# Kernel optimization log

Measured on AMD Instinct MI355X. Metric: run time of the kernel, lower is better.

Reference implementation:

```python
import jax, jax.numpy as jnp
import numpy as np

DIM = 128
HEADS = 4
DIM_HEAD = 32
HIDDEN = HEADS * DIM_HEAD  # 128
EPS = 1e-5


def setup_inputs() -> dict:
    key = jax.random.key(0)
    ks = jax.random.split(key, 5)
    x = jax.random.normal(ks[0], (32, DIM, 64, 64), dtype=jnp.float32)
    # 1x1 convs are channel matmuls
    Wqkv = jax.random.normal(ks[1], (HIDDEN * 3, DIM), dtype=jnp.float32) * (1.0 / np.sqrt(DIM))
    Wout = jax.random.normal(ks[2], (DIM, HIDDEN), dtype=jnp.float32) * (1.0 / np.sqrt(HIDDEN))
    bout = jnp.zeros((DIM,), dtype=jnp.float32)
    ln_w = jnp.ones((DIM,), dtype=jnp.float32)
    ln_b = jnp.zeros((DIM,), dtype=jnp.float32)
    return {"x": x, "Wqkv": Wqkv, "Wout": Wout, "bout": bout, "ln_w": ln_w, "ln_b": ln_b}


def reference(x, Wqkv, Wout, bout, ln_w, ln_b):
    b, c, h, w = x.shape
    n = h * w
    xf = x.reshape(b, c, n)  # b c n
    qkv = jnp.einsum('oc,bcn->bon', Wqkv, xf)  # b (3*hidden) n
    q, k, v = jnp.split(qkv, 3, axis=1)
    # b (h d) n -> b h d n
    q = q.reshape(b, HEADS, DIM_HEAD, n)
    k = k.reshape(b, HEADS, DIM_HEAD, n)
    v = v.reshape(b, HEADS, DIM_HEAD, n)
    q = jax.nn.softmax(q, axis=-2)  # over feature dim d
    k = jax.nn.softmax(k, axis=-1)  # over spatial dim n
    context = jnp.einsum('bhdn,bhen->bhde', k, v)
    out = jnp.einsum('bhde,bhdn->bhen', context, q)  # b h e n
    out = out.reshape(b, HIDDEN, n)
    out = jnp.einsum('oc,bcn->bon', Wout, out) + bout[None, :, None]
    out = out.reshape(b, DIM, h, w)
    # LayerNorm2d over channel dim, biased variance
    mean = jnp.mean(out, axis=1, keepdims=True)
    var = jnp.var(out, axis=1, keepdims=True)
    out = (out - mean) / jnp.sqrt(var + EPS) * ln_w[None, :, None, None] + ln_b[None, :, None, None]
    return out
```

## Files before the change

kernel.cpp:

```cpp
#include <hip/hip_runtime.h>
#include <stdint.h>


constexpr int B_   = 32;
constexpr int C_   = 128;
constexpr int N_   = 4096;
constexpr int NSUB = 8;
constexpr int TPB_ = 8;

using short8  = __attribute__((ext_vector_type(8))) short;
using short4v = __attribute__((ext_vector_type(4))) short;
using float4v = __attribute__((ext_vector_type(4))) float;

__device__ __forceinline__ unsigned short bf16_rne(float f) {
    union { float f; uint32_t u; } v; v.f = f;
    uint32_t u = v.u;
    u += 0x7FFFu + ((u >> 16) & 1u);
    return (unsigned short)(u >> 16);
}

constexpr size_t OFF_SP   = 0;
constexpr size_t OFF_CTXP = 131072;
constexpr size_t OFF_WBIG = 4325376;
constexpr size_t OFF_QSM  = 5373952;

__global__ __launch_bounds__(1024) void k1_qkv(const float* __restrict__ x,
                                               const float* __restrict__ Wqkv,
                                               unsigned short* __restrict__ qsm,
                                               float* __restrict__ ctx_part,
                                               float* __restrict__ S_part) {
    __shared__ __align__(16) unsigned short xs0[64 * 136];
    __shared__ __align__(16) unsigned short xs1[64 * 136];
    __shared__ __align__(16) unsigned short ek[128 * 72];
    __shared__ __align__(16) unsigned short vsh[128 * 72];

    const int b    = blockIdx.y;
    const int tblk = blockIdx.x;
    const int tid  = threadIdx.x;

    const int lane = tid & 63;
    const int wv   = tid >> 6;
    const int l15  = lane & 15;
    const int quad = lane >> 4;

    const float4v zero = {0.f, 0.f, 0.f, 0.f};

    short8 wfa[8];
    if (wv < 12) {
        const float* wqp = Wqkv + (wv * 32 + l15) * C_ + quad * 8;
        #pragma unroll
        for (int kk = 0; kk < 4; kk++) {
            float4v a0 = *(const float4v*)(wqp + kk * 32);
            float4v a1 = *(const float4v*)(wqp + kk * 32 + 4);
            float4v b0 = *(const float4v*)(wqp + 16 * C_ + kk * 32);
            float4v b1 = *(const float4v*)(wqp + 16 * C_ + kk * 32 + 4);
            short8 lo, hi;
            #pragma unroll
            for (int j = 0; j < 4; j++) {
                lo[j]     = (short)bf16_rne(a0[j]);
                lo[4 + j] = (short)bf16_rne(a1[j]);
                hi[j]     = (short)bf16_rne(b0[j]);
                hi[4 + j] = (short)bf16_rne(b1[j]);
            }
            wfa[kk]     = lo;
            wfa[4 + kk] = hi;
        }
    }

    const int sid = tid & 255;
    const int snl = sid & 63;
    const int scg = sid >> 6;
    const float* xbase = x + ((size_t)b * C_ + (size_t)scg * 32) * N_ + snl;
    float xv[32];
    short8 c16[4];
    auto load_x = [&](int s) {
        const float* xp = xbase + (tblk * NSUB + s) * 64;
        #pragma unroll
        for (int i = 0; i < 32; i++) xv[i] = xp[(size_t)i * N_];
    };
    auto conv_x = [&]() {
        #pragma unroll
        for (int ii = 0; ii < 4; ii++) {
            short8 v8;
            #pragma unroll
            for (int j = 0; j < 8; j++) v8[j] = (short)bf16_rne(xv[ii * 8 + j]);
            c16[ii] = v8;
        }
    };
    auto store_c = [&](unsigned short* xs) {
        unsigned short* dst = &xs[snl * 136 + scg * 32];
        #pragma unroll
        for (int ii = 0; ii < 4; ii++) *(short8*)(dst + ii * 8) = c16[ii];
    };

    if (wv >= 12) {
        load_x(0); conv_x(); store_c(xs0);
        load_x(1);
    }
    unsigned short* xs_cur = xs0;
    unsigned short* xs_nxt = xs1;

    float4v cacc = zero;
    float sk0[4] = {0.f, 0.f, 0.f, 0.f};
    float sk1[4] = {0.f, 0.f, 0.f, 0.f};
    const int ch  = wv >> 2;
    const int cdt = (wv >> 1) & 1;
    const int cet = wv & 1;

    for (int s = 0; s < NSUB; s++) {
        const int ns = (tblk * NSUB + s) * 64;
        __syncthreads();

        if (wv < 12) {
            #pragma unroll
            for (int ct = 0; ct < 4; ct++) {
                short8 bfx[4];
                #pragma unroll
                for (int kk = 0; kk < 4; kk++)
                    bfx[kk] = *(const short8*)&xs_cur[(ct * 16 + l15) * 136 + kk * 32 + quad * 8];
                float4v acc0 = zero, acc1 = zero;
                #pragma unroll
                for (int kk = 0; kk < 4; kk++) {
                    acc0 = __builtin_amdgcn_mfma_f32_16x16x32_bf16(wfa[kk],     bfx[kk], acc0, 0, 0, 0);
                    acc1 = __builtin_amdgcn_mfma_f32_16x16x32_bf16(wfa[4 + kk], bfx[kk], acc1, 0, 0, 0);
                }
                const int ncol = ct * 16 + l15;
                if (wv < 4) {
                    float e0[4], e1[4], z = 0.f;
                    #pragma unroll
                    for (int r = 0; r < 4; r++) {
                        e0[r] = __expf(acc0[r]); e1[r] = __expf(acc1[r]);
                        z += e0[r] + e1[r];
                    }
                    z += __shfl_xor(z, 16, 64);
                    z += __shfl_xor(z, 32, 64);
                    const float iz = 1.0f / z;
                    unsigned short* qp = qsm + ((size_t)b * N_ + ns + ncol) * C_ + wv * 32 + quad * 4;
                    short4v s0, s1;
                    #pragma unroll
                    for (int r = 0; r < 4; r++) {
                        s0[r] = (short)bf16_rne(e0[r] * iz);
                        s1[r] = (short)bf16_rne(e1[r] * iz);
                    }
                    *(short4v*)qp = s0;
                    *(short4v*)(qp + 16) = s1;
                } else if (wv < 8) {
                    const int row0 = (wv - 4) * 32 + quad * 4;
                    #pragma unroll
                    for (int r = 0; r < 4; r++) {
                        const float e0v = __expf(acc0[r]);
                        const float e1v = __expf(acc1[r]);
                        sk0[r] += e0v;
                        sk1[r] += e1v;
                        ek[(row0 + r) * 72 + ncol]      = bf16_rne(e0v);
                        ek[(row0 + 16 + r) * 72 + ncol] = bf16_rne(e1v);
                    }
                } else {
                    const int row0 = (wv - 8) * 32 + quad * 4;
                    #pragma unroll
                    for (int r = 0; r < 4; r++) {
                        vsh[(row0 + r) * 72 + ncol]      = bf16_rne(acc0[r]);
                        vsh[(row0 + 16 + r) * 72 + ncol] = bf16_rne(acc1[r]);
                    }
                }
            }
        } else {
            if (s + 1 < NSUB) { conv_x(); store_c(xs_nxt); }
            if (s + 2 < NSUB) load_x(s + 2);
        }
        __syncthreads();

        {
            const unsigned short* ap = &ek[(ch * 32 + cdt * 16 + l15) * 72 + quad * 8];
            const unsigned short* bp = &vsh[(ch * 32 + cet * 16 + l15) * 72 + quad * 8];
            #pragma unroll
            for (int kk = 0; kk < 2; kk++) {
                short8 a  = *(const short8*)(ap + kk * 32);
                short8 bb = *(const short8*)(bp + kk * 32);
                cacc = __builtin_amdgcn_mfma_f32_16x16x32_bf16(a, bb, cacc, 0, 0, 0);
            }
        }
        { unsigned short* t = xs_cur; xs_cur = xs_nxt; xs_nxt = t; }
    }

    {
        float* cp = ctx_part + ((size_t)(b * TPB_ + tblk) << 12)
                  + ((ch * 32 + cdt * 16 + quad * 4) * 32 + cet * 16 + l15);
        #pragma unroll
        for (int r = 0; r < 4; r++) cp[r * 32] = cacc[r];
    }
    if (wv >= 4 && wv < 8) {
        const int srow = (wv - 4) * 32 + quad * 4;
        float* sp = S_part + (size_t)(b * TPB_ + tblk) * 128;
        #pragma unroll
        for (int r = 0; r < 4; r++) {
            float a0 = sk0[r], a1 = sk1[r];
            a0 += __shfl_xor(a0, 1, 64); a0 += __shfl_xor(a0, 2, 64);
            a0 += __shfl_xor(a0, 4, 64); a0 += __shfl_xor(a0, 8, 64);
            a1 += __shfl_xor(a1, 1, 64); a1 += __shfl_xor(a1, 2, 64);
            a1 += __shfl_xor(a1, 4, 64); a1 += __shfl_xor(a1, 8, 64);
            if (l15 == 0) { sp[srow + r] = a0; sp[srow + 16 + r] = a1; }
        }
    }
}

__global__ __launch_bounds__(512) void k2_fused(const float* __restrict__ ctx_part,
                                                const float* __restrict__ S_part,
                                                const float* __restrict__ Wout,
                                                unsigned short* __restrict__ wbig) {
    __shared__ float Sinv[128];
    __shared__ __align__(16) unsigned short ctxb[128 * 40];
    const int b   = blockIdx.x;
    const int tid = threadIdx.x;

    if (tid < 128) {
        float s = 0.f;
        #pragma unroll
        for (int t = 0; t < TPB_; t++)
            s += S_part[(size_t)(b * TPB_ + t) * 128 + tid];
        Sinv[tid] = 1.0f / s;
    }
    __syncthreads();

    #pragma unroll
    for (int i = 0; i < 8; i++) {
        const int ei = i * 512 + tid;
        float v = 0.f;
        #pragma unroll
        for (int t = 0; t < TPB_; t++)
            v += ctx_part[((size_t)(b * TPB_ + t) << 12) + ei];
        ctxb[(ei >> 5) * 40 + (ei & 31)] = bf16_rne(v * Sinv[ei >> 5]);
    }
    __syncthreads();

    const int lane = tid & 63, wv = tid >> 6, l15 = lane & 15, quad = lane >> 4;
    const float4v zero = {0.f, 0.f, 0.f, 0.f};

    short8 a4[4];
    {
        const float* wop = Wout + (wv * 16 + l15) * C_ + quad * 8;
        #pragma unroll
        for (int h = 0; h < 4; h++) {
            float4v f0 = *(const float4v*)(wop + h * 32);
            float4v f1 = *(const float4v*)(wop + h * 32 + 4);
            short8 w;
            #pragma unroll
            for (int j = 0; j < 4; j++) {
                w[j]     = (short)bf16_rne(f0[j]);
                w[4 + j] = (short)bf16_rne(f1[j]);
            }
            a4[h] = w;
        }
    }

    unsigned short* wb = wbig + (size_t)b * (C_ * C_);
    #pragma unroll
    for (int ht = 0; ht < 8; ht++) {
        const int h_ = ht >> 1;
        short8 bb = *(const short8*)&ctxb[(h_ * 32 + (ht & 1) * 16 + l15) * 40 + quad * 8];
        float4v c4 = __builtin_amdgcn_mfma_f32_16x16x32_bf16(a4[h_], bb, zero, 0, 0, 0);
        const int c     = wv * 4 + (ht >> 1);
        const int quadp = (ht & 1) * 2 + (l15 >> 3);
        #pragma unroll
        for (int r = 0; r < 4; r++)
            wb[((c * 64 + quadp * 16 + quad * 4 + r) << 3) + (l15 & 7)] = bf16_rne(c4[r]);
    }
}

__global__ __launch_bounds__(512) void k3_out(const unsigned short* __restrict__ qsm,
                                              const unsigned short* __restrict__ wbig,
                                              const float* __restrict__ bout,
                                              const float* __restrict__ lnw,
                                              const float* __restrict__ lnb,
                                              float* __restrict__ out) {
    __shared__ __align__(16) unsigned short wls[16384];
    __shared__ float lnp[384];

    const int b    = blockIdx.y;
    const int tseg = blockIdx.x;
    const int tid  = threadIdx.x;

    const int lane = tid & 63, wv = tid >> 6, l15 = lane & 15, quad = lane >> 4;
    const int nl = wv * 16 + l15;

    const float4v zero = {0.f, 0.f, 0.f, 0.f};
    const size_t n0base = (size_t)tseg * 256;

    short8 st[4];
    {
        const short8* src = (const short8*)(wbig + (size_t)b * (C_ * C_));
        #pragma unroll
        for (int i = 0; i < 4; i++) st[i] = src[i * 512 + tid];
    }
    if (tid < 128) {
        lnp[tid]       = bout[tid];
        lnp[128 + tid] = lnw[tid];
        lnp[256 + tid] = lnb[tid];
    }
    short8 bq[4], bqn[4];
    {
        const unsigned short* qp = qsm + ((size_t)b * N_ + n0base + nl) * C_ + quad * 8;
        #pragma unroll
        for (int kk = 0; kk < 4; kk++) bq[kk] = *(const short8*)(qp + kk * 32);
    }
    #pragma unroll
    for (int i = 0; i < 4; i++)
        *(short8*)&wls[(i * 512 + tid) * 8] = st[i];
    __syncthreads();

    #pragma unroll
    for (int t = 0; t < 2; t++) {
        const size_t n = n0base + t * 128 + nl;
        if (t == 0) {
            const unsigned short* qp = qsm + ((size_t)b * N_ + n0base + 128 + nl) * C_ + quad * 8;
            #pragma unroll
            for (int kk = 0; kk < 4; kk++) bqn[kk] = *(const short8*)(qp + kk * 32);
        }

        float4v acc[8];
        #pragma unroll
        for (int ot = 0; ot < 8; ot++) {
            float4v a = zero;
            #pragma unroll
            for (int kk = 0; kk < 4; kk++) {
                short8 w = *(const short8*)&wls[((ot * 4 + kk) * 64 + lane) * 8];
                a = __builtin_amdgcn_mfma_f32_16x16x32_bf16(w, bq[kk], a, 0, 0, 0);
            }
            acc[ot] = a;
        }

        float sum = 0.f, sq = 0.f;
        #pragma unroll
        for (int ot = 0; ot < 8; ot++) {
            #pragma unroll
            for (int r = 0; r < 4; r++) {
                const int o = ot * 16 + quad * 4 + r;
                const float y = acc[ot][r] + lnp[o];
                acc[ot][r] = y;
                sum += y; sq += y * y;
            }
        }
        sum += __shfl_xor(sum, 16, 64);
        sum += __shfl_xor(sum, 32, 64);
        sq  += __shfl_xor(sq, 16, 64);
        sq  += __shfl_xor(sq, 32, 64);
        const float mean = sum * (1.0f / 128.0f);
        const float var  = sq * (1.0f / 128.0f) - mean * mean;
        const float rstd = rsqrtf(var + 1e-5f);

        #pragma unroll
        for (int ot = 0; ot < 8; ot++) {
            #pragma unroll
            for (int r = 0; r < 4; r++) {
                const int o = ot * 16 + quad * 4 + r;
                out[((size_t)b * C_ + o) * N_ + n] = (acc[ot][r] - mean) * rstd * lnp[128 + o] + lnp[256 + o];
            }
        }

        #pragma unroll
        for (int kk = 0; kk < 4; kk++) bq[kk] = bqn[kk];
    }
}

extern "C" void kernel_launch(void* const* d_in, const int* in_sizes, int n_in,
                              void* d_out, int out_size, void* d_ws, size_t ws_size,
                              hipStream_t stream) {
    const float* x    = (const float*)d_in[0];
    const float* Wqkv = (const float*)d_in[1];
    const float* Wout = (const float*)d_in[2];
    const float* bout = (const float*)d_in[3];
    const float* lnw  = (const float*)d_in[4];
    const float* lnb  = (const float*)d_in[5];
    float* out = (float*)d_out;

    char* ws = (char*)d_ws;
    float* S_part        = (float*)(ws + OFF_SP);
    float* ctx_part      = (float*)(ws + OFF_CTXP);
    unsigned short* wbig = (unsigned short*)(ws + OFF_WBIG);
    unsigned short* qsm  = (unsigned short*)(ws + OFF_QSM);

    k1_qkv<<<dim3(TPB_, B_), 1024, 0, stream>>>(x, Wqkv, qsm, ctx_part, S_part);
    k2_fused<<<B_, 512, 0, stream>>>(ctx_part, S_part, Wout, wbig);
    k3_out<<<dim3(16, B_), 512, 0, stream>>>(qsm, wbig, bout, lnw, lnb, out);
}
```

Before: 157.5 us.

## Retile QKV projection so each wave computes 64 rows by 32 columns

```diff
diff --git a/kernel.cpp b/kernel.cpp
--- a/kernel.cpp
+++ b/kernel.cpp
@@ -20,9 +20,9 @@
 }
 
 constexpr size_t OFF_SP   = 0;
-constexpr size_t OFF_CTXP = 131072;
-constexpr size_t OFF_WBIG = 4325376;
-constexpr size_t OFF_QSM  = 5373952;
+constexpr size_t OFF_CTXP = 262144;
+constexpr size_t OFF_WBIG = 4456448;
+constexpr size_t OFF_QSM  = 5505024;
 
 __global__ __launch_bounds__(1024) void k1_qkv(const float* __restrict__ x,
                                                const float* __restrict__ Wqkv,
@@ -45,25 +45,26 @@
 
     const float4v zero = {0.f, 0.f, 0.f, 0.f};
 
-    short8 wfa[8];
+    const int rg = wv >> 1;
+    const int cg = wv & 1;
+
+    short8 wfa[16];
     if (wv < 12) {
-        const float* wqp = Wqkv + (wv * 32 + l15) * C_ + quad * 8;
-        #pragma unroll
-        for (int kk = 0; kk < 4; kk++) {
-            float4v a0 = *(const float4v*)(wqp + kk * 32);
-            float4v a1 = *(const float4v*)(wqp + kk * 32 + 4);
-            float4v b0 = *(const float4v*)(wqp + 16 * C_ + kk * 32);
-            float4v b1 = *(const float4v*)(wqp + 16 * C_ + kk * 32 + 4);
-            short8 lo, hi;
-            #pragma unroll
-            for (int j = 0; j < 4; j++) {
-                lo[j]     = (short)bf16_rne(a0[j]);
-                lo[4 + j] = (short)bf16_rne(a1[j]);
-                hi[j]     = (short)bf16_rne(b0[j]);
-                hi[4 + j] = (short)bf16_rne(b1[j]);
-            }
-            wfa[kk]     = lo;
-            wfa[4 + kk] = hi;
+        const float* wqp = Wqkv + ((size_t)(rg * 64 + l15)) * C_ + quad * 8;
+        #pragma unroll
+        for (int rt = 0; rt < 4; rt++) {
+            #pragma unroll
+            for (int kk = 0; kk < 4; kk++) {
+                float4v f0 = *(const float4v*)(wqp + rt * 16 * C_ + kk * 32);
+                float4v f1 = *(const float4v*)(wqp + rt * 16 * C_ + kk * 32 + 4);
+                short8 w;
+                #pragma unroll
+                for (int j = 0; j < 4; j++) {
+                    w[j]     = (short)bf16_rne(f0[j]);
+                    w[4 + j] = (short)bf16_rne(f1[j]);
+                }
+                wfa[rt * 4 + kk] = w;
+            }
         }
     }
 
@@ -101,8 +102,7 @@
     unsigned short* xs_nxt = xs1;
 
     float4v cacc = zero;
-    float sk0[4] = {0.f, 0.f, 0.f, 0.f};
-    float sk1[4] = {0.f, 0.f, 0.f, 0.f};
+    float sk[16] = {0.f};
     const int ch  = wv >> 2;
     const int cdt = (wv >> 1) & 1;
     const int cet = wv & 1;
@@ -113,55 +113,63 @@
 
         if (wv < 12) {
             #pragma unroll
-            for (int ct = 0; ct < 4; ct++) {
+            for (int c = 0; c < 2; c++) {
+                const int ct = cg * 2 + c;
                 short8 bfx[4];
                 #pragma unroll
                 for (int kk = 0; kk < 4; kk++)
                     bfx[kk] = *(const short8*)&xs_cur[(ct * 16 + l15) * 136 + kk * 32 + quad * 8];
-                float4v acc0 = zero, acc1 = zero;
+                float4v acc[4] = {zero, zero, zero, zero};
                 #pragma unroll
                 for (int kk = 0; kk < 4; kk++) {
-                    acc0 = __builtin_amdgcn_mfma_f32_16x16x32_bf16(wfa[kk],     bfx[kk], acc0, 0, 0, 0);
-                    acc1 = __builtin_amdgcn_mfma_f32_16x16x32_bf16(wfa[4 + kk], bfx[kk], acc1, 0, 0, 0);
+                    acc[0] = __builtin_amdgcn_mfma_f32_16x16x32_bf16(wfa[kk],      bfx[kk], acc[0], 0, 0, 0);
+                    acc[1] = __builtin_amdgcn_mfma_f32_16x16x32_bf16(wfa[4 + kk],  bfx[kk], acc[1], 0, 0, 0);
+                    acc[2] = __builtin_amdgcn_mfma_f32_16x16x32_bf16(wfa[8 + kk],  bfx[kk], acc[2], 0, 0, 0);
+                    acc[3] = __builtin_amdgcn_mfma_f32_16x16x32_bf16(wfa[12 + kk], bfx[kk], acc[3], 0, 0, 0);
                 }
                 const int ncol = ct * 16 + l15;
-                if (wv < 4) {
-                    float e0[4], e1[4], z = 0.f;
+                if (rg < 2) {
                     #pragma unroll
-                    for (int r = 0; r < 4; r++) {
-                        e0[r] = __expf(acc0[r]); e1[r] = __expf(acc1[r]);
-                        z += e0[r] + e1[r];
+                    for (int hh = 0; hh < 2; hh++) {
+                        float e[8], z = 0.f;
+                        #pragma unroll
+                        for (int t = 0; t < 2; t++)
+                            #pragma unroll
+                            for (int r = 0; r < 4; r++) {
+                                e[t * 4 + r] = __expf(acc[hh * 2 + t][r]);
+                                z += e[t * 4 + r];
+                            }
+                        z += __shfl_xor(z, 16, 64);
+                        z += __shfl_xor(z, 32, 64);
+                        const float iz = 1.0f / z;
+                        unsigned short* qp = qsm + ((size_t)b * N_ + ns + ncol) * C_
+                                           + (rg * 2 + hh) * 32 + quad * 4;
+                        short4v s0, s1;
+                        #pragma unroll
+                        for (int r = 0; r < 4; r++) {
+                            s0[r] = (short)bf16_rne(e[r] * iz);
+                            s1[r] = (short)bf16_rne(e[4 + r] * iz);
+                        }
+                        *(short4v*)qp = s0;
+                        *(short4v*)(qp + 16) = s1;
                     }
-                    z += __shfl_xor(z, 16, 64);
-                    z += __shfl_xor(z, 32, 64);
-                    const float iz = 1.0f / z;
-                    unsigned short* qp = qsm + ((size_t)b * N_ + ns + ncol) * C_ + wv * 32 + quad * 4;
-                    short4v s0, s1;
+                } else if (rg < 4) {
+                    const int row0 = (rg - 2) * 64 + quad * 4;
                     #pragma unroll
-                    for (int r = 0; r < 4; r++) {
-                        s0[r] = (short)bf16_rne(e0[r] * iz);
-                        s1[r] = (short)bf16_rne(e1[r] * iz);
-                    }
-                    *(short4v*)qp = s0;
-                    *(short4v*)(qp + 16) = s1;
-                } else if (wv < 8) {
-                    const int row0 = (wv - 4) * 32 + quad * 4;
+                    for (int rt = 0; rt < 4; rt++)
+                        #pragma unroll
+                        for (int r = 0; r < 4; r++) {
+                            const float ev = __expf(acc[rt][r]);
+                            sk[rt * 4 + r] += ev;
+                            ek[(row0 + rt * 16 + r) * 72 + ncol] = bf16_rne(ev);
+                        }
+                } else {
+                    const int row0 = (rg - 4) * 64 + quad * 4;
                     #pragma unroll
-                    for (int r = 0; r < 4; r++) {
-                        const float e0v = __expf(acc0[r]);
-                        const float e1v = __expf(acc1[r]);
-                        sk0[r] += e0v;
-                        sk1[r] += e1v;
-                        ek[(row0 + r) * 72 + ncol]      = bf16_rne(e0v);
-                        ek[(row0 + 16 + r) * 72 + ncol] = bf16_rne(e1v);
-                    }
-                } else {
-                    const int row0 = (wv - 8) * 32 + quad * 4;
-                    #pragma unroll
-                    for (int r = 0; r < 4; r++) {
-                        vsh[(row0 + r) * 72 + ncol]      = bf16_rne(acc0[r]);
-                        vsh[(row0 + 16 + r) * 72 + ncol] = bf16_rne(acc1[r]);
-                    }
+                    for (int rt = 0; rt < 4; rt++)
+                        #pragma unroll
+                        for (int r = 0; r < 4; r++)
+                            vsh[(row0 + rt * 16 + r) * 72 + ncol] = bf16_rne(acc[rt][r]);
                 }
             }
         } else {
@@ -189,18 +197,17 @@
         #pragma unroll
         for (int r = 0; r < 4; r++) cp[r * 32] = cacc[r];
     }
-    if (wv >= 4 && wv < 8) {
-        const int srow = (wv - 4) * 32 + quad * 4;
-        float* sp = S_part + (size_t)(b * TPB_ + tblk) * 128;
-        #pragma unroll
-        for (int r = 0; r < 4; r++) {
-            float a0 = sk0[r], a1 = sk1[r];
-            a0 += __shfl_xor(a0, 1, 64); a0 += __shfl_xor(a0, 2, 64);
-            a0 += __shfl_xor(a0, 4, 64); a0 += __shfl_xor(a0, 8, 64);
-            a1 += __shfl_xor(a1, 1, 64); a1 += __shfl_xor(a1, 2, 64);
-            a1 += __shfl_xor(a1, 4, 64); a1 += __shfl_xor(a1, 8, 64);
-            if (l15 == 0) { sp[srow + r] = a0; sp[srow + 16 + r] = a1; }
-        }
+    if (rg == 2 || rg == 3) {
+        float* sp = S_part + (((size_t)(b * TPB_ + tblk) * 2 + cg)) * 128 + (rg - 2) * 64;
+        #pragma unroll
+        for (int rt = 0; rt < 4; rt++)
+            #pragma unroll
+            for (int r = 0; r < 4; r++) {
+                float a = sk[rt * 4 + r];
+                a += __shfl_xor(a, 1, 64); a += __shfl_xor(a, 2, 64);
+                a += __shfl_xor(a, 4, 64); a += __shfl_xor(a, 8, 64);
+                if (l15 == 0) sp[rt * 16 + quad * 4 + r] = a;
+            }
     }
 }
 
@@ -216,8 +223,8 @@
     if (tid < 128) {
         float s = 0.f;
         #pragma unroll
-        for (int t = 0; t < TPB_; t++)
-            s += S_part[(size_t)(b * TPB_ + t) * 128 + tid];
+        for (int t = 0; t < 16; t++)
+            s += S_part[((size_t)b * 16 + t) * 128 + tid];
         Sinv[tid] = 1.0f / s;
     }
     __syncthreads();
```

New measurement: 233.6 us. +48.3%, slower.
